# Kernel optimization log

Hardware: AMD Instinct MI355X
Metric: run time of the kernel (lower is better)

## Reference

```python
import jax, jax.numpy as jnp
import numpy as np

B, D, T, V = 16, 128, 4096, 1024


def setup_inputs() -> dict:
    key = jax.random.key(0)
    k1, k2 = jax.random.split(key)
    latents = jax.random.normal(k1, (B, D, T), dtype=jnp.float32)
    codebook = jax.random.normal(k2, (V, D), dtype=jnp.float32)  # code_embed.weight
    return {"latents": latents, "codebook": codebook}


def reference(latents, codebook):
    # decode(): latents (B, D, T) -> (B, T, D); nearest code under L2 (torch.cdist + argmin)
    x = jnp.transpose(latents, (0, 2, 1))  # (B, T, D)
    x_sq = jnp.sum(x * x, axis=-1, keepdims=True)          # (B, T, 1)
    c_sq = jnp.sum(codebook * codebook, axis=-1)           # (V,)
    cross = jnp.einsum('btd,vd->btv', x, codebook)         # (B, T, V) -- the fusion target
    d2 = x_sq - 2.0 * cross + c_sq                         # (B, T, V)
    codes = jnp.argmin(d2, axis=-1)                        # (B, T) int
    # quantized latents: embed the chosen codes back to (B, D, T)
    quantized = jnp.transpose(codebook[codes], (0, 2, 1))  # (B, D, T)
    return codes.astype(jnp.int32), quantized
```

## Files before the change

### kernel.cpp

```cpp
#include <hip/hip_runtime.h>

#define B_ 16
#define D_ 128
#define T_ 4096
#define V_ 1024

typedef _Float16 half8 __attribute__((ext_vector_type(8)));
typedef float float4v __attribute__((ext_vector_type(4)));


__global__ __launch_bounds__(256) void split_csq_kernel(const float* __restrict__ cb,
                                                        _Float16* __restrict__ Bh,
                                                        _Float16* __restrict__ Bl,
                                                        float* __restrict__ chsq) {
    const int g = blockIdx.x * 256 + threadIdx.x;
    const int v = g >> 4;
    const int k0 = (g & 15) << 3;
    const float* src = cb + (size_t)v * D_ + k0;
    half8 h, l;
    float s = 0.f;
#pragma unroll
    for (int j = 0; j < 8; ++j) {
        float c = src[j];
        _Float16 ch = (_Float16)c;
        h[j] = ch;
        l[j] = (_Float16)((c - (float)ch) * 2048.0f);
        s = fmaf(c, c, s);
    }
    const int kt = k0 >> 5;
    const int kk = k0 & 31;
    const size_t off = ((size_t)(kt * V_ + v)) * 32 + kk;
    *(half8*)(Bh + off) = h;
    *(half8*)(Bl + off) = l;
#pragma unroll
    for (int o = 1; o < 16; o <<= 1) s += __shfl_xor(s, o, 64);
    if ((g & 15) == 0) chsq[v] = 0.5f * s;
}

__device__ __forceinline__ void dma16(const char* g, char* lds) {
    __builtin_amdgcn_global_load_lds(
        (const __attribute__((address_space(1))) unsigned int*)g,
        (__attribute__((address_space(3))) unsigned int*)lds, 16, 0, 0);
}

__device__ __forceinline__ void dma_chunk(char* ldsbuf, const char* BhB, const char* BlB,
                                          int c, int wq, int tl) {
#pragma unroll
    for (int j = 0; j < 4; ++j) {
        const int seg = wq * 4 + j;
        const int hl = seg >> 3;
        const int kt = (seg >> 1) & 3;
        const int o1k = seg & 1;
        const char* src = (hl ? BlB : BhB) + kt * 65536 + c * 2048 + o1k * 1024 + tl * 16;
        dma16(src, ldsbuf + seg * 1024);
    }
}

__global__ __launch_bounds__(256, 2) void vq_mfma(const float* __restrict__ latents,
                                                  const float* __restrict__ codebook,
                                                  const float* __restrict__ chsq,
                                                  const _Float16* __restrict__ Bh,
                                                  const _Float16* __restrict__ Bl,
                                                  float* __restrict__ out_codes,
                                                  float* __restrict__ out_q) {
    __shared__ __align__(16) char smem[69632];
    __shared__ float sChsq[V_];
    __shared__ int scode[128];

    const int tid = threadIdx.x;
    const int tl = tid & 63;
    const int wq = tid >> 6;
    const int ln = tid & 15;
    const int q = (tid >> 4) & 3;
    const int b = blockIdx.x >> 5;
    const int t00 = (blockIdx.x & 31) << 7;

    _Float16* AhS = (_Float16*)smem;
    _Float16* AlS = AhS + 128 * 136;

#pragma unroll
    for (int i = 0; i < V_ / 256; ++i) sChsq[tid + i * 256] = chsq[tid + i * 256];

#pragma unroll
    for (int th = 0; th < 2; ++th) {
        const int row = th * 64 + tl;
        const float* xp = latents + (size_t)b * D_ * T_ + t00 + row;
#pragma unroll
        for (int i = 0; i < 4; ++i) {
            const int d0 = wq * 32 + i * 8;
            float x[8];
#pragma unroll
            for (int j = 0; j < 8; ++j) x[j] = xp[(size_t)(d0 + j) * T_];
            half8 h, l;
#pragma unroll
            for (int j = 0; j < 8; ++j) {
                _Float16 xh = (_Float16)x[j];
                h[j] = xh;
                l[j] = (_Float16)((x[j] - (float)xh) * 2048.0f);
            }
            *(half8*)(AhS + row * 136 + d0) = h;
            *(half8*)(AlS + row * 136 + d0) = l;
        }
    }
    __syncthreads();

    half8 ah[4][2], al[4][2];
#pragma unroll
    for (int kt = 0; kt < 4; ++kt)
#pragma unroll
        for (int mt = 0; mt < 2; ++mt) {
            const int row = wq * 32 + mt * 16 + ln;
            ah[kt][mt] = *(const half8*)(AhS + row * 136 + kt * 32 + q * 8);
            al[kt][mt] = *(const half8*)(AlS + row * 136 + kt * 32 + q * 8);
        }
    __syncthreads();

    char* Bb = smem;
    const char* BhB = (const char*)Bh;
    const char* BlB = (const char*)Bl;

    float bestF[2][4];
    int bestv[2][4];
#pragma unroll
    for (int mt = 0; mt < 2; ++mt)
#pragma unroll
        for (int r = 0; r < 4; ++r) {
            bestF[mt][r] = 3.0e38f;
            bestv[mt][r] = 0;
        }

    dma_chunk(Bb, BhB, BlB, 0, wq, tl);
    __syncthreads();

    for (int c = 0; c < 32; ++c) {
        if (c + 1 < 32) dma_chunk(Bb + ((c + 1) & 1) * 16384, BhB, BlB, c + 1, wq, tl);

        const char* buf = Bb + (c & 1) * 16384;
        float4v acc1[2][2], acc2[2][2];
#pragma unroll
        for (int mt = 0; mt < 2; ++mt)
#pragma unroll
            for (int ntl = 0; ntl < 2; ++ntl) {
                acc1[mt][ntl] = (float4v){0.f, 0.f, 0.f, 0.f};
                acc2[mt][ntl] = (float4v){0.f, 0.f, 0.f, 0.f};
            }
#pragma unroll
        for (int kt = 0; kt < 4; ++kt) {
            half8 bh[2], bl[2];
#pragma unroll
            for (int ntl = 0; ntl < 2; ++ntl) {
                const int o = kt * 2048 + (ntl * 16 + ln) * 64 + q * 16;
                bh[ntl] = *(const half8*)(buf + o);
                bl[ntl] = *(const half8*)(buf + 8192 + o);
            }
#pragma unroll
            for (int ntl = 0; ntl < 2; ++ntl)
#pragma unroll
                for (int mt = 0; mt < 2; ++mt) {
                    acc1[mt][ntl] = __builtin_amdgcn_mfma_f32_16x16x32_f16(
                        ah[kt][mt], bh[ntl], acc1[mt][ntl], 0, 0, 0);
                    acc2[mt][ntl] = __builtin_amdgcn_mfma_f32_16x16x32_f16(
                        ah[kt][mt], bl[ntl], acc2[mt][ntl], 0, 0, 0);
                    acc2[mt][ntl] = __builtin_amdgcn_mfma_f32_16x16x32_f16(
                        al[kt][mt], bh[ntl], acc2[mt][ntl], 0, 0, 0);
                }
        }
#pragma unroll
        for (int ntl = 0; ntl < 2; ++ntl) {
            const int n = c * 32 + ntl * 16 + ln;
            const float csq = sChsq[n];
#pragma unroll
            for (int mt = 0; mt < 2; ++mt)
#pragma unroll
                for (int r = 0; r < 4; ++r) {
                    const float score =
                        csq - (acc1[mt][ntl][r] + acc2[mt][ntl][r] * (1.0f / 2048.0f));
                    if (score < bestF[mt][r]) {
                        bestF[mt][r] = score;
                        bestv[mt][r] = n;
                    }
                }
        }
        __syncthreads();
    }

#pragma unroll
    for (int off = 1; off < 16; off <<= 1) {
#pragma unroll
        for (int mt = 0; mt < 2; ++mt)
#pragma unroll
            for (int r = 0; r < 4; ++r) {
                const float of = __shfl_xor(bestF[mt][r], off, 64);
                const int ov = __shfl_xor(bestv[mt][r], off, 64);
                if (of < bestF[mt][r] || (of == bestF[mt][r] && ov < bestv[mt][r])) {
                    bestF[mt][r] = of;
                    bestv[mt][r] = ov;
                }
            }
    }

    if (ln == 0) {
#pragma unroll
        for (int mt = 0; mt < 2; ++mt)
#pragma unroll
            for (int r = 0; r < 4; ++r) {
                const int m = wq * 32 + mt * 16 + q * 4 + r;
                scode[m] = bestv[mt][r];
                out_codes[(size_t)b * T_ + t00 + m] = (float)bestv[mt][r];
            }
    }
    __syncthreads();

#pragma unroll
    for (int th = 0; th < 2; ++th) {
        const int row = th * 64 + tl;
        const int code = scode[row];
        const float* crow = codebook + (size_t)code * D_;
        float* qp = out_q + (size_t)b * D_ * T_ + t00 + row;
#pragma unroll
        for (int i = 0; i < 32; ++i) {
            const int d = wq * 32 + i;
            qp[(size_t)d * T_] = crow[d];
        }
    }
}

extern "C" void kernel_launch(void* const* d_in, const int* in_sizes, int n_in,
                              void* d_out, int out_size, void* d_ws, size_t ws_size,
                              hipStream_t stream) {
    const float* latents = (const float*)d_in[0];
    const float* codebook = (const float*)d_in[1];

    float* out_codes = (float*)d_out;
    float* out_q = (float*)d_out + B_ * T_;

    float* chsq = (float*)d_ws;
    _Float16* Bh = (_Float16*)((char*)d_ws + 4096);
    _Float16* Bl = (_Float16*)((char*)d_ws + 4096 + 262144);

    split_csq_kernel<<<(V_ * 16) / 256, 256, 0, stream>>>(codebook, Bh, Bl, chsq);
    vq_mfma<<<(B_ * T_) / 128, 256, 0, stream>>>(latents, codebook, chsq, Bh, Bl,
                                                 out_codes, out_q);
}
```

Measured before the change: 130.3 us.

## Pre-swizzle codebook chunks for contiguous DMA and defer argmin fold one chunk

The codebook split kernel now writes hi/lo fp16 halves in a chunk-contiguous, MFMA-fragment-ordered layout. Each chunk DMA becomes one contiguous copy, and LDS fragment reads become lane-linear (tl*16), which avoids strided bank patterns. The accumulators are double-buffered so the score/argmin fold for chunk c-1 runs after chunk c's MFMAs are issued, overlapping VALU compare work with matrix work. The cost is twice the accumulator registers, which may pressure the two-waves-per-SIMD occupancy target.

```diff
diff --git a/kernel.cpp b/kernel.cpp
--- a/kernel.cpp
+++ b/kernel.cpp
@@ -10,8 +10,7 @@
 
 
 __global__ __launch_bounds__(256) void split_csq_kernel(const float* __restrict__ cb,
-                                                        _Float16* __restrict__ Bh,
-                                                        _Float16* __restrict__ Bl,
+                                                        char* __restrict__ Bc,
                                                         float* __restrict__ chsq) {
     const int g = blockIdx.x * 256 + threadIdx.x;
     const int v = g >> 4;
@@ -28,10 +27,14 @@
         s = fmaf(c, c, s);
     }
     const int kt = k0 >> 5;
-    const int kk = k0 & 31;
-    const size_t off = ((size_t)(kt * V_ + v)) * 32 + kk;
-    *(half8*)(Bh + off) = h;
-    *(half8*)(Bl + off) = l;
+    const int q = (k0 >> 3) & 3;
+    const int c = v >> 5;
+    const int ntl = (v >> 4) & 1;
+    const int ln = v & 15;
+    const size_t off =
+        (size_t)c * 16384 + kt * 2048 + ntl * 1024 + (size_t)(q * 16 + ln) * 16;
+    *(half8*)(Bc + off) = h;
+    *(half8*)(Bc + off + 8192) = l;
 #pragma unroll
     for (int o = 1; o < 16; o <<= 1) s += __shfl_xor(s, o, 64);
     if ((g & 15) == 0) chsq[v] = 0.5f * s;
@@ -43,24 +46,19 @@
         (__attribute__((address_space(3))) unsigned int*)lds, 16, 0, 0);
 }
 
-__device__ __forceinline__ void dma_chunk(char* ldsbuf, const char* BhB, const char* BlB,
-                                          int c, int wq, int tl) {
+__device__ __forceinline__ void dma_chunk(char* ldsbuf, const char* Bc, int c, int wq,
+                                          int tl) {
 #pragma unroll
     for (int j = 0; j < 4; ++j) {
         const int seg = wq * 4 + j;
-        const int hl = seg >> 3;
-        const int kt = (seg >> 1) & 3;
-        const int o1k = seg & 1;
-        const char* src = (hl ? BlB : BhB) + kt * 65536 + c * 2048 + o1k * 1024 + tl * 16;
-        dma16(src, ldsbuf + seg * 1024);
+        dma16(Bc + (size_t)c * 16384 + seg * 1024 + tl * 16, ldsbuf + seg * 1024);
     }
 }
 
 __global__ __launch_bounds__(256, 2) void vq_mfma(const float* __restrict__ latents,
                                                   const float* __restrict__ codebook,
                                                   const float* __restrict__ chsq,
-                                                  const _Float16* __restrict__ Bh,
-                                                  const _Float16* __restrict__ Bl,
+                                                  const char* __restrict__ Bc,
                                                   float* __restrict__ out_codes,
                                                   float* __restrict__ out_q) {
     __shared__ __align__(16) char smem[69632];
@@ -116,8 +114,6 @@
     __syncthreads();
 
     char* Bb = smem;
-    const char* BhB = (const char*)Bh;
-    const char* BlB = (const char*)Bl;
 
     float bestF[2][4];
     int bestv[2][4];
@@ -129,60 +125,67 @@
             bestv[mt][r] = 0;
         }
 
-    dma_chunk(Bb, BhB, BlB, 0, wq, tl);
-    __syncthreads();
-
-    for (int c = 0; c < 32; ++c) {
-        if (c + 1 < 32) dma_chunk(Bb + ((c + 1) & 1) * 16384, BhB, BlB, c + 1, wq, tl);
-
-        const char* buf = Bb + (c & 1) * 16384;
-        float4v acc1[2][2], acc2[2][2];
-#pragma unroll
-        for (int mt = 0; mt < 2; ++mt)
-#pragma unroll
-            for (int ntl = 0; ntl < 2; ++ntl) {
-                acc1[mt][ntl] = (float4v){0.f, 0.f, 0.f, 0.f};
-                acc2[mt][ntl] = (float4v){0.f, 0.f, 0.f, 0.f};
-            }
-#pragma unroll
-        for (int kt = 0; kt < 4; ++kt) {
-            half8 bh[2], bl[2];
-#pragma unroll
-            for (int ntl = 0; ntl < 2; ++ntl) {
-                const int o = kt * 2048 + (ntl * 16 + ln) * 64 + q * 16;
-                bh[ntl] = *(const half8*)(buf + o);
-                bl[ntl] = *(const half8*)(buf + 8192 + o);
-            }
-#pragma unroll
-            for (int ntl = 0; ntl < 2; ++ntl)
-#pragma unroll
-                for (int mt = 0; mt < 2; ++mt) {
-                    acc1[mt][ntl] = __builtin_amdgcn_mfma_f32_16x16x32_f16(
-                        ah[kt][mt], bh[ntl], acc1[mt][ntl], 0, 0, 0);
-                    acc2[mt][ntl] = __builtin_amdgcn_mfma_f32_16x16x32_f16(
-                        ah[kt][mt], bl[ntl], acc2[mt][ntl], 0, 0, 0);
-                    acc2[mt][ntl] = __builtin_amdgcn_mfma_f32_16x16x32_f16(
-                        al[kt][mt], bh[ntl], acc2[mt][ntl], 0, 0, 0);
-                }
-        }
+    float4v acc1[2][2][2], acc2[2][2][2];
+
+    auto fold = [&](int s, int cc) {
 #pragma unroll
         for (int ntl = 0; ntl < 2; ++ntl) {
-            const int n = c * 32 + ntl * 16 + ln;
+            const int n = cc * 32 + ntl * 16 + ln;
             const float csq = sChsq[n];
 #pragma unroll
             for (int mt = 0; mt < 2; ++mt)
 #pragma unroll
                 for (int r = 0; r < 4; ++r) {
-                    const float score =
-                        csq - (acc1[mt][ntl][r] + acc2[mt][ntl][r] * (1.0f / 2048.0f));
+                    const float score = csq - (acc1[s][mt][ntl][r] +
+                                               acc2[s][mt][ntl][r] * (1.0f / 2048.0f));
                     if (score < bestF[mt][r]) {
                         bestF[mt][r] = score;
                         bestv[mt][r] = n;
                     }
                 }
         }
+    };
+
+    dma_chunk(Bb, Bc, 0, wq, tl);
+    __syncthreads();
+
+    for (int c = 0; c < 32; ++c) {
+        const int set = c & 1;
+        if (c + 1 < 32) dma_chunk(Bb + ((c + 1) & 1) * 16384, Bc, c + 1, wq, tl);
+
+        const char* buf = Bb + set * 16384;
+#pragma unroll
+        for (int mt = 0; mt < 2; ++mt)
+#pragma unroll
+            for (int ntl = 0; ntl < 2; ++ntl) {
+                acc1[set][mt][ntl] = (float4v){0.f, 0.f, 0.f, 0.f};
+                acc2[set][mt][ntl] = (float4v){0.f, 0.f, 0.f, 0.f};
+            }
+#pragma unroll
+        for (int kt = 0; kt < 4; ++kt) {
+            half8 bh[2], bl[2];
+#pragma unroll
+            for (int ntl = 0; ntl < 2; ++ntl) {
+                const int o = kt * 2048 + ntl * 1024 + tl * 16;
+                bh[ntl] = *(const half8*)(buf + o);
+                bl[ntl] = *(const half8*)(buf + 8192 + o);
+            }
+#pragma unroll
+            for (int ntl = 0; ntl < 2; ++ntl)
+#pragma unroll
+                for (int mt = 0; mt < 2; ++mt) {
+                    acc1[set][mt][ntl] = __builtin_amdgcn_mfma_f32_16x16x32_f16(
+                        ah[kt][mt], bh[ntl], acc1[set][mt][ntl], 0, 0, 0);
+                    acc2[set][mt][ntl] = __builtin_amdgcn_mfma_f32_16x16x32_f16(
+                        ah[kt][mt], bl[ntl], acc2[set][mt][ntl], 0, 0, 0);
+                    acc2[set][mt][ntl] = __builtin_amdgcn_mfma_f32_16x16x32_f16(
+                        al[kt][mt], bh[ntl], acc2[set][mt][ntl], 0, 0, 0);
+                }
+        }
+        if (c > 0) fold(set ^ 1, c - 1);
         __syncthreads();
     }
+    fold(1, 31);
 
 #pragma unroll
     for (int off = 1; off < 16; off <<= 1) {
@@ -235,10 +238,9 @@
     float* out_q = (float*)d_out + B_ * T_;
 
     float* chsq = (float*)d_ws;
-    _Float16* Bh = (_Float16*)((char*)d_ws + 4096);
-    _Float16* Bl = (_Float16*)((char*)d_ws + 4096 + 262144);
-
-    split_csq_kernel<<<(V_ * 16) / 256, 256, 0, stream>>>(codebook, Bh, Bl, chsq);
-    vq_mfma<<<(B_ * T_) / 128, 256, 0, stream>>>(latents, codebook, chsq, Bh, Bl,
-                                                 out_codes, out_q);
-}
+    char* Bc = (char*)d_ws + 4096;
+
+    split_csq_kernel<<<(V_ * 16) / 256, 256, 0, stream>>>(codebook, Bc, chsq);
+    vq_mfma<<<(B_ * T_) / 128, 256, 0, stream>>>(latents, codebook, chsq, Bc, out_codes,
+                                                 out_q);
+}
```

Result: slower. 138.9 us (+6.6%).
